# Kernel tuning notes

Measured on AMD Instinct MI355X. Metric: run time of the kernel, lower is better.

The kernel has to match this reference:

```python
import jax, jax.numpy as jnp
import numpy as np

GAMMA = 10.0  # kernel bandwidth (init arg gamma)

def setup_inputs() -> dict:
    key = jax.random.key(0)
    k1, k2, k3, k4 = jax.random.split(key, 4)
    n_train, n_test, d, n_cls = 16384, 8192, 3072, 10
    return {
        "x_train": jax.random.normal(k1, (n_train, d), dtype=jnp.float32),
        "y_train": jax.random.normal(k2, (n_train, n_cls), dtype=jnp.float32),
        "x_test": jax.random.normal(k3, (n_test, d), dtype=jnp.float32),
        "M": jax.random.normal(k4, (d, d), dtype=jnp.float32),
    }

def reference(x_train, y_train, x_test, M):
    # Mahalanobis squared distances: ||s||_M^2 - 2 s M c^T + ||c||_M^2
    sM = x_train @ M                              # [n_train, d]
    s_norm2 = (sM * x_train).sum(-1)              # [n_train]
    c_norm2 = ((x_test @ M) * x_test).sum(-1)     # [n_test]
    d2 = (-2.0) * (sM @ x_test.T) + s_norm2[:, None] + c_norm2[None, :]
    dist = jnp.sqrt(jnp.clip(d2, 0.0))            # laplacian uses non-squared dist
    K = jnp.exp(dist * (-1.0 / GAMMA))            # [n_train, n_test]
    Kt = K.T                                      # [n_test, n_train]
    normalized = Kt / Kt.sum(axis=1, keepdims=True)
    out = normalized @ y_train                    # [n_test, n_cls]
    return (out, M)
```

## Files before the change

kernel.cpp:

```cpp
#include <hip/hip_runtime.h>
#include <hip/hip_bf16.h>

#define D_DIM 3072
#define NTRAIN 16384
#define NTEST 8192

typedef __attribute__((ext_vector_type(4))) float f32x4;
typedef __attribute__((ext_vector_type(4))) int i32x4;
typedef __attribute__((ext_vector_type(8))) int i32x8;

__device__ __forceinline__ unsigned short f2bf(float f) {
  union { float f; unsigned u; } x; x.f = f;
  unsigned r = x.u + 0x7FFFu + ((x.u >> 16) & 1u);
  return (unsigned short)(r >> 16);
}

__device__ __forceinline__ float bf2f(unsigned short b) {
  union { unsigned u; float f; } x; x.u = ((unsigned)b) << 16;
  return x.f;
}

__device__ __forceinline__ i32x8 cmb(i32x4 lo, i32x4 hi) {
  i32x8 r;
  r[0] = lo[0]; r[1] = lo[1]; r[2] = lo[2]; r[3] = lo[3];
  r[4] = hi[0]; r[5] = hi[1]; r[6] = hi[2]; r[7] = hi[3];
  return r;
}

__device__ __forceinline__ void gload16(const void* g, void* l) {
  __builtin_amdgcn_global_load_lds(
      (const __attribute__((address_space(1))) void*)g,
      (__attribute__((address_space(3))) void*)l, 16, 0, 0);
}

__device__ __forceinline__ void swz_tile(int& tileY, int& tileX) {
  const int gx = gridDim.x, gy = gridDim.y;
  const int L = blockIdx.y * gx + blockIdx.x;
  const int q = (gx * gy) >> 3;
  const int s = (L & 7) * q + (L >> 3);
  const int sid = s >> 6;
  const int t = s & 63;
  const int scols = gx >> 3;
  const int sy = sid / scols, sx = sid - sy * scols;
  tileY = sy * 8 + (t >> 3);
  tileX = sx * 8 + (t & 7);
}

__device__ __forceinline__ void swz_lin(int& tileY, int& tileX) {
  const int gx = gridDim.x;
  const int nwg = gx * gridDim.y;
  const int L = blockIdx.y * gx + blockIdx.x;
  const int s = (L & 7) * (nwg >> 3) + (L >> 3);
  tileY = s / gx;
  tileX = s - tileY * gx;
}

__global__ void k_convert8(const float* __restrict__ in, unsigned char* __restrict__ out, long n8) {
  long i = (long)blockIdx.x * blockDim.x + threadIdx.x;
  long stride = (long)gridDim.x * blockDim.x;
  for (; i < n8; i += stride) {
    float4 a = reinterpret_cast<const float4*>(in)[i * 2];
    float4 b = reinterpret_cast<const float4*>(in)[i * 2 + 1];
    int w0 = __builtin_amdgcn_cvt_pk_fp8_f32(a.x, a.y, 0, false);
    w0 = __builtin_amdgcn_cvt_pk_fp8_f32(a.z, a.w, w0, true);
    int w1 = __builtin_amdgcn_cvt_pk_fp8_f32(b.x, b.y, 0, false);
    w1 = __builtin_amdgcn_cvt_pk_fp8_f32(b.z, b.w, w1, true);
    reinterpret_cast<int2*>(out)[i] = make_int2(w0, w1);
  }
}

__global__ void k_copy4(const float4* __restrict__ in, float4* __restrict__ out, long n4) {
  long i = (long)blockIdx.x * blockDim.x + threadIdx.x;
  long stride = (long)gridDim.x * blockDim.x;
  for (; i < n4; i += stride) out[i] = in[i];
}

__global__ void k_transpose_fp8(const float* __restrict__ M, unsigned char* __restrict__ Mt) {
  __shared__ float t[32][33];
  int bx = blockIdx.x * 32, by = blockIdx.y * 32;
  int tx = threadIdx.x, ty = threadIdx.y;
#pragma unroll
  for (int i = 0; i < 32; i += 8)
    t[ty + i][tx] = M[(size_t)(by + ty + i) * D_DIM + bx + tx];
  __syncthreads();
#pragma unroll
  for (int i = 0; i < 32; i += 8) {
    float v = t[tx][ty + i];
    int p = __builtin_amdgcn_cvt_pk_fp8_f32(v, v, 0, false);
    Mt[(size_t)(bx + ty + i) * D_DIM + by + tx] = (unsigned char)(p & 0xFF);
  }
}

__device__ __forceinline__ void mainloop4ph(const unsigned char* __restrict__ ga,
                                            const unsigned char* __restrict__ gb,
                                            unsigned char* As, unsigned char* Bs,
                                            int aRow0, int bRow0, int lhi, int tid,
                                            f32x4 acc[8][4]) {
  const int nt = D_DIM / 128;
#pragma unroll
  for (int j = 0; j < 4; ++j) {
    gload16(ga + (size_t)j * 64 * D_DIM, As + j * 8192 + tid * 16);
    gload16(gb + (size_t)j * 64 * D_DIM, Bs + j * 8192 + tid * 16);
  }
  const int g0 = lhi, g1 = lhi ^ 4;
  for (int t = 0; t < nt; ++t) {
    const int p = t & 1;
    const unsigned char* Ac = As + p * 32768;
    const unsigned char* Bc = Bs + p * 32768;
    unsigned char* An = As + (p ^ 1) * 32768;
    unsigned char* Bn = Bs + (p ^ 1) * 32768;
    const bool stage = (t + 1 < nt);
    const int k1 = (t + 1) * 128;
    asm volatile("s_waitcnt vmcnt(0)" ::: "memory");
    __builtin_amdgcn_s_barrier();
    __builtin_amdgcn_sched_barrier(0);
    if (stage) {
#pragma unroll
      for (int j = 0; j < 4; ++j) {
        gload16(ga + (size_t)j * 64 * D_DIM + k1, An + j * 8192 + tid * 16);
        gload16(gb + (size_t)j * 64 * D_DIM + k1, Bn + j * 8192 + tid * 16);
      }
    }

#define RDA(q, H)                                                                    \
  cmb(*reinterpret_cast<const i32x4*>(                                               \
          &Ac[(aRow0 + (q) * 32 + (H) * 16) * 128 +                                  \
              ((g0 ^ ((aRow0 + (q) * 32 + (H) * 16) & 7)) * 16)]),                   \
      *reinterpret_cast<const i32x4*>(                                               \
          &Ac[(aRow0 + (q) * 32 + (H) * 16) * 128 +                                  \
              ((g1 ^ ((aRow0 + (q) * 32 + (H) * 16) & 7)) * 16)]))

#define MFMA8(q, A0, A1)                                                             \
  __builtin_amdgcn_s_setprio(1);                                                     \
  _Pragma("unroll") for (int n = 0; n < 4; ++n) {                                    \
    acc[(q) * 2][n] = __builtin_amdgcn_mfma_scale_f32_16x16x128_f8f6f4(              \
        A0, b8[n], acc[(q) * 2][n], 0, 0, 0, 127, 0, 127);                           \
    acc[(q) * 2 + 1][n] = __builtin_amdgcn_mfma_scale_f32_16x16x128_f8f6f4(          \
        A1, b8[n], acc[(q) * 2 + 1][n], 0, 0, 0, 127, 0, 127);                       \
  }                                                                                  \
  __builtin_amdgcn_s_setprio(0);                                                     \
  __builtin_amdgcn_sched_barrier(0);

    i32x8 b8[4];
#pragma unroll
    for (int n = 0; n < 4; ++n) {
      const int row = bRow0 + n * 16;
      const int f = row & 7;
      b8[n] = cmb(*reinterpret_cast<const i32x4*>(&Bc[row * 128 + ((g0 ^ f) * 16)]),
                  *reinterpret_cast<const i32x4*>(&Bc[row * 128 + ((g1 ^ f) * 16)]));
    }
    i32x8 a0 = RDA(0, 0), a1 = RDA(0, 1);
    __builtin_amdgcn_sched_barrier(0);
    i32x8 p0 = RDA(1, 0), p1 = RDA(1, 1);
    MFMA8(0, a0, a1)
    a0 = RDA(2, 0); a1 = RDA(2, 1);
    MFMA8(1, p0, p1)
    p0 = RDA(3, 0); p1 = RDA(3, 1);
    MFMA8(2, a0, a1)
    MFMA8(3, p0, p1)
#undef RDA
#undef MFMA8
  }
}

template <bool WRITE_SM>
__global__ __launch_bounds__(512, 2) void k_gemm_xm8(const unsigned char* __restrict__ X8,
                                                     const unsigned char* __restrict__ Mt8,
                                                     const float* __restrict__ Xf,
                                                     unsigned char* __restrict__ smOut,
                                                     float* __restrict__ norm) {
  __shared__ unsigned char As[2 * 256 * 128], Bs[2 * 256 * 128];
  const int tid = threadIdx.x, lane = tid & 63, wave = tid >> 6;
  const int wm = wave >> 2, wn = wave & 3;
  const int l15 = lane & 15, lhi = lane >> 4;
  int tileY, tileX;
  swz_lin(tileY, tileX);
  const int rowBase = tileY * 256, colBase = tileX * 256;
  const int srow = tid >> 3, ssl = tid & 7;
  const unsigned char* ga = X8 + (size_t)(rowBase + srow) * D_DIM + ((ssl ^ (srow & 7)) * 16);
  const unsigned char* gb = Mt8 + (size_t)(colBase + srow) * D_DIM + ((ssl ^ (srow & 7)) * 16);
  f32x4 acc[8][4] = {};
  mainloop4ph(ga, gb, As, Bs, wm * 128 + l15, wn * 64 + l15, lhi, tid, acc);
  __syncthreads();

  const int c0 = colBase + wn * 64 + l15;
#pragma unroll
  for (int m = 0; m < 8; ++m) {
#pragma unroll
    for (int r = 0; r < 4; ++r) {
      const size_t grow = rowBase + wm * 128 + m * 16 + lhi * 4 + r;
      float v = 0.f;
#pragma unroll
      for (int n = 0; n < 4; ++n) {
        float a = acc[m][n][r];
        const int gcol = c0 + n * 16;
        v += a * Xf[grow * D_DIM + gcol];
        if (WRITE_SM) {
          int pk = __builtin_amdgcn_cvt_pk_fp8_f32(a, a, 0, false);
          smOut[grow * D_DIM + gcol] = (unsigned char)(pk & 0xFF);
        }
      }
      v += __shfl_xor(v, 1); v += __shfl_xor(v, 2);
      v += __shfl_xor(v, 4); v += __shfl_xor(v, 8);
      if ((lane & 15) == 0) atomicAdd(&norm[grow], v);
    }
  }
}

__global__ __launch_bounds__(512, 2) void k_gemm_cross(const unsigned char* __restrict__ sM8,
                                                       const unsigned char* __restrict__ xte8h,
                                                       const float* __restrict__ sn2,
                                                       const float* __restrict__ cn2h,
                                                       unsigned short* __restrict__ S) {
  __shared__ unsigned char As[2 * 256 * 128], Bs[2 * 256 * 128];
  const int tid = threadIdx.x, lane = tid & 63, wave = tid >> 6;
  const int wm = wave >> 2, wn = wave & 3;
  const int l15 = lane & 15, lhi = lane >> 4;
  int tileY, tileX;
  swz_tile(tileY, tileX);
  const int rowBase = tileY * 256, colBase = tileX * 256;
  const int srow = tid >> 3, ssl = tid & 7;
  const unsigned char* ga = sM8 + (size_t)(rowBase + srow) * D_DIM + ((ssl ^ (srow & 7)) * 16);
  const unsigned char* gb = xte8h + (size_t)(colBase + srow) * D_DIM + ((ssl ^ (srow & 7)) * 16);
  const int bRow0 = wn * 64 + l15;
  f32x4 acc[8][4] = {};
  mainloop4ph(ga, gb, As, Bs, wm * 128 + l15, bRow0, lhi, tid, acc);
  __syncthreads();

  float* snlds = reinterpret_cast<float*>(As);
  if (tid < 256) snlds[tid] = sn2[rowBase + tid];
  __syncthreads();
  float cn[4];
#pragma unroll
  for (int n = 0; n < 4; ++n) cn[n] = cn2h[colBase + bRow0 + n * 16];
#pragma unroll
  for (int m = 0; m < 8; ++m) {
#pragma unroll
    for (int r = 0; r < 4; ++r) {
      const int lrow = wm * 128 + m * 16 + lhi * 4 + r;
      const float sn = snlds[lrow];
      const size_t grow = rowBase + lrow;
#pragma unroll
      for (int n = 0; n < 4; ++n) {
        float d2 = sn + cn[n] - 2.f * acc[m][n][r];
        float kv = exp2f(-0.14426950408889634f * sqrtf(fmaxf(d2, 0.f)));
        S[grow * 4096 + colBase + bRow0 + n * 16] = f2bf(kv);
      }
    }
  }
}

__global__ __launch_bounds__(256) void k_out(const unsigned short* __restrict__ S,
                                             const float* __restrict__ Y,
                                             float* __restrict__ part, int halfBase) {
  __shared__ float ylds[256 * 10];
  const int tid = threadIdx.x;
  const int sBase = blockIdx.y * 256;
  const int tloc = blockIdx.x * 256 + tid;
  const int tglob = halfBase + tloc;
  for (int i = tid; i < 2560; i += 256) ylds[i] = Y[(size_t)sBase * 10 + i];
  __syncthreads();
  float num[10] = {0, 0, 0, 0, 0, 0, 0, 0, 0, 0};
  float den = 0.f;
  for (int s = 0; s < 256; ++s) {
    float kv = bf2f(S[(size_t)(sBase + s) * 4096 + tloc]);
    const float* yr = &ylds[s * 10];
#pragma unroll
    for (int c = 0; c < 10; ++c) num[c] += kv * yr[c];
    den += kv;
  }
#pragma unroll
  for (int c = 0; c < 10; ++c)
    part[((size_t)blockIdx.y * 11 + c) * NTEST + tglob] = num[c];
  part[((size_t)blockIdx.y * 11 + 10) * NTEST + tglob] = den;
}

__global__ void k_reduce(const float* __restrict__ part, float* __restrict__ out) {
  int t = blockIdx.x * blockDim.x + threadIdx.x;
  float num[10] = {0, 0, 0, 0, 0, 0, 0, 0, 0, 0};
  float den = 0.f;
  for (int it = 0; it < NTRAIN / 256; ++it) {
    const float* p = part + (size_t)it * 11 * NTEST + t;
#pragma unroll
    for (int c = 0; c < 10; ++c) num[c] += p[(size_t)c * NTEST];
    den += p[(size_t)10 * NTEST];
  }
  float inv = 1.f / den;
#pragma unroll
  for (int c = 0; c < 10; ++c) out[(size_t)t * 10 + c] = num[c] * inv;
}

extern "C" void kernel_launch(void* const* d_in, const int* in_sizes, int n_in,
                              void* d_out, int out_size, void* d_ws, size_t ws_size,
                              hipStream_t stream) {
  const float* x_train = (const float*)d_in[0];
  const float* y_train = (const float*)d_in[1];
  const float* x_test  = (const float*)d_in[2];
  const float* M       = (const float*)d_in[3];
  float* out = (float*)d_out;

  char* ws = (char*)d_ws;
  unsigned char*  xtr8 = (unsigned char*)(ws + 0);
  unsigned char*  xte8 = (unsigned char*)(ws + 50331648);
  unsigned char*  Mt8  = (unsigned char*)(ws + 75497472);
  unsigned char*  sM8  = (unsigned char*)(ws + 84934656);
  float* s_n2 = (float*)(ws + 135266304);
  float* c_n2 = (float*)(ws + 135331840);
  float* part = (float*)(ws + 135364608);
  unsigned short* S = (unsigned short*)(ws + 158433280);

  hipMemsetAsync(ws + 135266304, 0, 98304, stream);

  k_convert8<<<1024, 256, 0, stream>>>(x_train, xtr8, (long)NTRAIN * D_DIM / 8);
  k_convert8<<<1024, 256, 0, stream>>>(x_test, xte8, (long)NTEST * D_DIM / 8);
  k_transpose_fp8<<<dim3(96, 96), dim3(32, 8), 0, stream>>>(M, Mt8);
  k_copy4<<<2048, 256, 0, stream>>>((const float4*)M, (float4*)(out + 81920),
                                    (long)D_DIM * D_DIM / 4);

  k_gemm_xm8<true><<<dim3(12, 64), 512, 0, stream>>>(xtr8, Mt8, x_train, sM8, s_n2);
  k_gemm_xm8<false><<<dim3(12, 32), 512, 0, stream>>>(xte8, Mt8, x_test, nullptr, c_n2);

  for (int h = 0; h < 2; ++h) {
    k_gemm_cross<<<dim3(16, 64), 512, 0, stream>>>(
        sM8, xte8 + (size_t)h * 4096 * D_DIM, s_n2, c_n2 + h * 4096, S);
    k_out<<<dim3(16, 64), 256, 0, stream>>>(S, y_train, part, h * 4096);
  }
  k_reduce<<<32, 256, 0, stream>>>(part, out);
}
```

Before: 1.055 ms.

## Load B operand fragments directly from global into registers, dropping B LDS staging

The FP8 GEMM main loop no longer stages the B tile through shared memory. Each wave loads its own B fragments straight from global memory into registers, double-buffered across two unrolled tile bodies, while A keeps its LDS double buffer. This halves LDS use and removes the B LDS writes and reads, which could allow more occupancy. In exchange, B reads are no longer shared across the two wm waves, so global and L2 traffic for B doubles, and the synchronous register loads may stall the MFMAs.

```diff
diff --git a/kernel.cpp b/kernel.cpp
--- a/kernel.cpp
+++ b/kernel.cpp
@@ -91,76 +91,72 @@
   }
 }
 
-__device__ __forceinline__ void mainloop4ph(const unsigned char* __restrict__ ga,
-                                            const unsigned char* __restrict__ gb,
-                                            unsigned char* As, unsigned char* Bs,
-                                            int aRow0, int bRow0, int lhi, int tid,
-                                            f32x4 acc[8][4]) {
+__device__ __forceinline__ void mainloopBG(const unsigned char* __restrict__ ga,
+                                           const unsigned char* __restrict__ gB,
+                                           unsigned char* As,
+                                           int aRow0, int bAbs0, int lhi, int tid,
+                                           f32x4 acc[8][4]) {
   const int nt = D_DIM / 128;
-#pragma unroll
-  for (int j = 0; j < 4; ++j) {
+  const int g0 = lhi, g1 = lhi ^ 4;
+  const unsigned char* pB0 = gB + (size_t)(bAbs0)*D_DIM;
+  const unsigned char* pB1 = gB + (size_t)(bAbs0 + 16) * D_DIM;
+  const unsigned char* pB2 = gB + (size_t)(bAbs0 + 32) * D_DIM;
+  const unsigned char* pB3 = gB + (size_t)(bAbs0 + 48) * D_DIM;
+#pragma unroll
+  for (int j = 0; j < 4; ++j)
     gload16(ga + (size_t)j * 64 * D_DIM, As + j * 8192 + tid * 16);
-    gload16(gb + (size_t)j * 64 * D_DIM, Bs + j * 8192 + tid * 16);
-  }
-  const int g0 = lhi, g1 = lhi ^ 4;
-  for (int t = 0; t < nt; ++t) {
-    const int p = t & 1;
-    const unsigned char* Ac = As + p * 32768;
-    const unsigned char* Bc = Bs + p * 32768;
-    unsigned char* An = As + (p ^ 1) * 32768;
-    unsigned char* Bn = Bs + (p ^ 1) * 32768;
-    const bool stage = (t + 1 < nt);
-    const int k1 = (t + 1) * 128;
-    asm volatile("s_waitcnt vmcnt(0)" ::: "memory");
-    __builtin_amdgcn_s_barrier();
-    __builtin_amdgcn_sched_barrier(0);
-    if (stage) {
-#pragma unroll
-      for (int j = 0; j < 4; ++j) {
-        gload16(ga + (size_t)j * 64 * D_DIM + k1, An + j * 8192 + tid * 16);
-        gload16(gb + (size_t)j * 64 * D_DIM + k1, Bn + j * 8192 + tid * 16);
-      }
-    }
-
-#define RDA(q, H)                                                                    \
+  i32x8 bA[4], bB[4];
+  bA[0] = cmb(*(const i32x4*)(pB0 + g0 * 16), *(const i32x4*)(pB0 + g1 * 16));
+  bA[1] = cmb(*(const i32x4*)(pB1 + g0 * 16), *(const i32x4*)(pB1 + g1 * 16));
+  bA[2] = cmb(*(const i32x4*)(pB2 + g0 * 16), *(const i32x4*)(pB2 + g1 * 16));
+  bA[3] = cmb(*(const i32x4*)(pB3 + g0 * 16), *(const i32x4*)(pB3 + g1 * 16));
+
+#define RDA(Ac, q, H)                                                                \
   cmb(*reinterpret_cast<const i32x4*>(                                               \
-          &Ac[(aRow0 + (q) * 32 + (H) * 16) * 128 +                                  \
-              ((g0 ^ ((aRow0 + (q) * 32 + (H) * 16) & 7)) * 16)]),                   \
+          &(Ac)[(aRow0 + (q) * 32 + (H) * 16) * 128 +                                \
+                ((g0 ^ ((aRow0 + (q) * 32 + (H) * 16) & 7)) * 16)]),                 \
       *reinterpret_cast<const i32x4*>(                                               \
-          &Ac[(aRow0 + (q) * 32 + (H) * 16) * 128 +                                  \
-              ((g1 ^ ((aRow0 + (q) * 32 + (H) * 16) & 7)) * 16)]))
-
-#define MFMA8(q, A0, A1)                                                             \
-  __builtin_amdgcn_s_setprio(1);                                                     \
-  _Pragma("unroll") for (int n = 0; n < 4; ++n) {                                    \
-    acc[(q) * 2][n] = __builtin_amdgcn_mfma_scale_f32_16x16x128_f8f6f4(              \
-        A0, b8[n], acc[(q) * 2][n], 0, 0, 0, 127, 0, 127);                           \
-    acc[(q) * 2 + 1][n] = __builtin_amdgcn_mfma_scale_f32_16x16x128_f8f6f4(          \
-        A1, b8[n], acc[(q) * 2 + 1][n], 0, 0, 0, 127, 0, 127);                       \
-  }                                                                                  \
-  __builtin_amdgcn_s_setprio(0);                                                     \
-  __builtin_amdgcn_sched_barrier(0);
-
-    i32x8 b8[4];
-#pragma unroll
-    for (int n = 0; n < 4; ++n) {
-      const int row = bRow0 + n * 16;
-      const int f = row & 7;
-      b8[n] = cmb(*reinterpret_cast<const i32x4*>(&Bc[row * 128 + ((g0 ^ f) * 16)]),
-                  *reinterpret_cast<const i32x4*>(&Bc[row * 128 + ((g1 ^ f) * 16)]));
-    }
-    i32x8 a0 = RDA(0, 0), a1 = RDA(0, 1);
-    __builtin_amdgcn_sched_barrier(0);
-    i32x8 p0 = RDA(1, 0), p1 = RDA(1, 1);
-    MFMA8(0, a0, a1)
-    a0 = RDA(2, 0); a1 = RDA(2, 1);
-    MFMA8(1, p0, p1)
-    p0 = RDA(3, 0); p1 = RDA(3, 1);
-    MFMA8(2, a0, a1)
-    MFMA8(3, p0, p1)
+          &(Ac)[(aRow0 + (q) * 32 + (H) * 16) * 128 +                                \
+                ((g1 ^ ((aRow0 + (q) * 32 + (H) * 16) & 7)) * 16)]))
+
+#define TILEBODY(par, bNow, bNxt)                                                    \
+  {                                                                                  \
+    const int t = tt + (par);                                                        \
+    const unsigned char* Ac = As + (par) * 32768;                                    \
+    unsigned char* An = As + ((par) ^ 1) * 32768;                                    \
+    asm volatile("s_waitcnt vmcnt(0)" ::: "memory");                                 \
+    __builtin_amdgcn_s_barrier();                                                    \
+    __builtin_amdgcn_sched_barrier(0);                                               \
+    if (t + 1 < nt) {                                                                \
+      const int k1 = (t + 1) * 128;                                                  \
+      _Pragma("unroll") for (int j = 0; j < 4; ++j)                                  \
+        gload16(ga + (size_t)j * 64 * D_DIM + k1, An + j * 8192 + tid * 16);         \
+      bNxt[0] = cmb(*(const i32x4*)(pB0 + k1 + g0 * 16), *(const i32x4*)(pB0 + k1 + g1 * 16)); \
+      bNxt[1] = cmb(*(const i32x4*)(pB1 + k1 + g0 * 16), *(const i32x4*)(pB1 + k1 + g1 * 16)); \
+      bNxt[2] = cmb(*(const i32x4*)(pB2 + k1 + g0 * 16), *(const i32x4*)(pB2 + k1 + g1 * 16)); \
+      bNxt[3] = cmb(*(const i32x4*)(pB3 + k1 + g0 * 16), *(const i32x4*)(pB3 + k1 + g1 * 16)); \
+    }                                                                                \
+    __builtin_amdgcn_sched_barrier(0);                                               \
+    _Pragma("unroll") for (int q = 0; q < 4; ++q) {                                  \
+      i32x8 a0 = RDA(Ac, q, 0), a1 = RDA(Ac, q, 1);                                  \
+      __builtin_amdgcn_s_setprio(1);                                                 \
+      _Pragma("unroll") for (int n = 0; n < 4; ++n) {                                \
+        acc[q * 2][n] = __builtin_amdgcn_mfma_scale_f32_16x16x128_f8f6f4(            \
+            a0, bNow[n], acc[q * 2][n], 0, 0, 0, 127, 0, 127);                       \
+        acc[q * 2 + 1][n] = __builtin_amdgcn_mfma_scale_f32_16x16x128_f8f6f4(        \
+            a1, bNow[n], acc[q * 2 + 1][n], 0, 0, 0, 127, 0, 127);                   \
+      }                                                                              \
+      __builtin_amdgcn_s_setprio(0);                                                 \
+      __builtin_amdgcn_sched_barrier(0);                                             \
+    }                                                                                \
+  }
+
+  for (int tt = 0; tt < nt; tt += 2) {
+    TILEBODY(0, bA, bB)
+    TILEBODY(1, bB, bA)
+  }
+#undef TILEBODY
 #undef RDA
-#undef MFMA8
-  }
 }
 
 template <bool WRITE_SM>
@@ -169,7 +165,7 @@
                                                      const float* __restrict__ Xf,
                                                      unsigned char* __restrict__ smOut,
                                                      float* __restrict__ norm) {
-  __shared__ unsigned char As[2 * 256 * 128], Bs[2 * 256 * 128];
+  __shared__ unsigned char As[2 * 256 * 128];
   const int tid = threadIdx.x, lane = tid & 63, wave = tid >> 6;
   const int wm = wave >> 2, wn = wave & 3;
   const int l15 = lane & 15, lhi = lane >> 4;
@@ -178,9 +174,8 @@
   const int rowBase = tileY * 256, colBase = tileX * 256;
   const int srow = tid >> 3, ssl = tid & 7;
   const unsigned char* ga = X8 + (size_t)(rowBase + srow) * D_DIM + ((ssl ^ (srow & 7)) * 16);
-  const unsigned char* gb = Mt8 + (size_t)(colBase + srow) * D_DIM + ((ssl ^ (srow & 7)) * 16);
   f32x4 acc[8][4] = {};
-  mainloop4ph(ga, gb, As, Bs, wm * 128 + l15, wn * 64 + l15, lhi, tid, acc);
+  mainloopBG(ga, Mt8, As, wm * 128 + l15, colBase + wn * 64 + l15, lhi, tid, acc);
   __syncthreads();
 
   const int c0 = colBase + wn * 64 + l15;
@@ -212,7 +207,7 @@
                                                        const float* __restrict__ sn2,
                                                        const float* __restrict__ cn2h,
                                                        unsigned short* __restrict__ S) {
-  __shared__ unsigned char As[2 * 256 * 128], Bs[2 * 256 * 128];
+  __shared__ unsigned char As[2 * 256 * 128];
   const int tid = threadIdx.x, lane = tid & 63, wave = tid >> 6;
   const int wm = wave >> 2, wn = wave & 3;
   const int l15 = lane & 15, lhi = lane >> 4;
@@ -221,10 +216,9 @@
   const int rowBase = tileY * 256, colBase = tileX * 256;
   const int srow = tid >> 3, ssl = tid & 7;
   const unsigned char* ga = sM8 + (size_t)(rowBase + srow) * D_DIM + ((ssl ^ (srow & 7)) * 16);
-  const unsigned char* gb = xte8h + (size_t)(colBase + srow) * D_DIM + ((ssl ^ (srow & 7)) * 16);
   const int bRow0 = wn * 64 + l15;
   f32x4 acc[8][4] = {};
-  mainloop4ph(ga, gb, As, Bs, wm * 128 + l15, bRow0, lhi, tid, acc);
+  mainloopBG(ga, xte8h, As, wm * 128 + l15, colBase + bRow0, lhi, tid, acc);
   __syncthreads();
 
   float* snlds = reinterpret_cast<float*>(As);
```

Result: slower. 2.556 ms (+142.2%).
